# Kernel tuning notes

Measured on AMD Instinct MI355X. Metric: run time of the kernel, lower is better.

Reference implementation:

```python
import jax, jax.numpy as jnp
import numpy as np
from jax import lax

EPS = 1e-12

V, D, L, B = 50000, 128, 2048, 64
K1, K2 = 64, 64
W1, W2, W3 = 8, 8, 8


def conv1d_same(x, w):
    # x: [B, L, Cin], w: [W, Cin, Cout] -> [B, L, Cout]
    return lax.conv_general_dilated(x, w, window_strides=(1,), padding='SAME',
                                    dimension_numbers=('NWC', 'WIO', 'NWC'))


def gru_final_state(x, Wx, Wh, b):
    # Keras GRU (reset_after=True, gate order z, r, h); returns final hidden state.
    # x: [B, L, D] -> h_T: [B, K2]
    U = Wh.shape[0]
    x_proj = jnp.einsum('bld,dk->blk', x, Wx) + b[0]  # [B, L, 3U]

    def step(h, xp_t):
        hp = h @ Wh + b[1]                       # [B, 3U]
        xz, xr, xh = jnp.split(xp_t, 3, axis=-1)
        hz, hr, hh_ = jnp.split(hp, 3, axis=-1)
        z = jax.nn.sigmoid(xz + hz)
        r = jax.nn.sigmoid(xr + hr)
        hh = jnp.tanh(xh + r * hh_)
        h_new = z * h + (1.0 - z) * hh
        return h_new, None

    h0 = jnp.zeros((x.shape[0], U), dtype=x.dtype)
    h_T, _ = lax.scan(step, h0, jnp.swapaxes(x_proj, 0, 1))
    return h_T


def setup_inputs() -> dict:
    key = jax.random.key(0)
    ks = jax.random.split(key, 10)
    s = 0.05
    return {
        'code_block': jax.random.randint(ks[0], (B, L), 0, V, dtype=jnp.int32),
        'E': jax.random.normal(ks[1], (V, D), jnp.float32) * s,
        'bias_table': jax.random.normal(ks[2], (V, 1), jnp.float32) * s,
        'Wx': jax.random.normal(ks[3], (D, 3 * K2), jnp.float32) * s,
        'Wh': jax.random.normal(ks[4], (K2, 3 * K2), jnp.float32) * s,
        'b_gru': jnp.zeros((2, 3 * K2), jnp.float32),
        'c1w': jax.random.normal(ks[5], (W1, D, K1), jnp.float32) * s,
        'c1b': jnp.zeros((K1,), jnp.float32),
        'c2w': jax.random.normal(ks[6], (W2, K1, K2), jnp.float32) * s,
        'c2b': jnp.zeros((K2,), jnp.float32),
        'c3w': jax.random.normal(ks[7], (W3, K2, 1), jnp.float32) * s,
        'c3b': jnp.zeros((1,), jnp.float32),
    }


def reference(code_block, E, bias_table, Wx, Wh, b_gru, c1w, c1b, c2w, c2b, c3w, c3b):
    tok = E[code_block]                          # [B, L, D] embedding gather
    bias = bias_table[code_block][..., 0]        # [B, L] per-token bias

    h_t = gru_final_state(tok, Wx, Wh, b_gru)    # [B, K2]

    # AttentionFeatures: conv -> relu -> conv -> * h_t -> l2-normalize (dropout off)
    L1 = jax.nn.relu(conv1d_same(tok, c1w) + c1b)        # [B, L, K1]
    L2 = (conv1d_same(L1, c2w) + c2b) * h_t[:, None, :]  # [B, L, K2]
    L_feat = L2 * lax.rsqrt(jnp.sum(L2 * L2, axis=-1, keepdims=True) + EPS)

    # AttentionWeights: conv to 1 channel, softmax over time
    a_logits = conv1d_same(L_feat, c3w)[..., 0] + c3b    # [B, L]
    alpha = jax.nn.softmax(a_logits, axis=-1)            # [B, L]

    # n_hat = sum_l alpha_l * embed_l
    n_hat = jnp.einsum('bl,bld->bd', alpha, tok)         # [B, D]

    # logits_l = <embed_l, n_hat> + bias_l ; softmax over positions
    logits = jnp.einsum('bld,bd->bl', tok, n_hat) + bias # [B, L]
    return jax.nn.softmax(logits, axis=-1)
```

## Files before the change

### kernel.cpp

```cpp
#include <hip/hip_runtime.h>

#define B_ 64
#define L_ 2048
#define D_ 128
#define LP 2056
#define PAD 3

typedef __attribute__((ext_vector_type(8))) short short8;
typedef __attribute__((ext_vector_type(4))) float f32x4;
typedef __attribute__((ext_vector_type(4))) unsigned short us4;

static __device__ __forceinline__ float bf2f(unsigned short u) {
  return __uint_as_float(((unsigned int)u) << 16);
}
static __device__ __forceinline__ unsigned short f2bf(float f) {
  unsigned int x = __float_as_uint(f);
  unsigned int r = (x + 0x7fffu + ((x >> 16) & 1u)) >> 16;
  return (unsigned short)r;
}

__global__ __launch_bounds__(256) void k_prep(
    const int* __restrict__ code, const float* __restrict__ bias_table,
    const float* __restrict__ Wx, const float* __restrict__ c1w,
    const float* __restrict__ c2w,
    unsigned short* __restrict__ tokpad, unsigned short* __restrict__ WxT,
    unsigned short* __restrict__ c1wT, unsigned short* __restrict__ c2wT,
    float* __restrict__ biasg)
{
  int id = blockIdx.x * 256 + threadIdx.x;
  const int NB = B_ * L_;
  if (id < NB) { biasg[id] = bias_table[code[id]]; return; }
  id -= NB;
  const int N3 = 192 * 128;
  if (id < N3) { int c = id >> 7, d = id & 127; WxT[id] = f2bf(Wx[d * 192 + c]); return; }
  id -= N3;
  const int N4 = 8 * 64 * 128;
  if (id < N4) {
    int w = id >> 13, c = (id >> 7) & 63, d = id & 127;
    c1wT[id] = f2bf(c1w[(w * 128 + d) * 64 + c]); return;
  }
  id -= N4;
  const int N5 = 8 * 64 * 64;
  if (id < N5) {
    int w = id >> 12, c = (id >> 6) & 63, d = id & 63;
    c2wT[id] = f2bf(c2w[(w * 64 + d) * 64 + c]); return;
  }
  id -= N5;
  if (id < 8192) {
    int b = id >> 7, rem = id & 127;
    int rr = rem >> 4, c8 = rem & 15;
    int row = (rr < 3) ? rr : (2051 + rr - 3);
    uint4 z = {0u, 0u, 0u, 0u};
    ((uint4*)tokpad)[(b * LP + row) * 16 + c8] = z;
  }
}

__global__ __launch_bounds__(256) void k_xproj(
    const int* __restrict__ code, const float* __restrict__ E,
    const unsigned short* __restrict__ WxT, const float* __restrict__ bg,
    unsigned short* __restrict__ tokpad, unsigned short* __restrict__ xg)
{
  __shared__ __align__(16) unsigned short At[128 * 136];
  __shared__ __align__(16) unsigned short Bt[192 * 136];
  __shared__ int codes[128];
  int b = blockIdx.x >> 4;
  int l0 = (blockIdx.x & 15) << 7;
  int tid = threadIdx.x;
  if (tid < 128) codes[tid] = code[b * L_ + l0 + tid];
  __syncthreads();
  for (int i = tid; i < 128 * 16; i += 256) {
    int row = i >> 4, c8 = i & 15;
    const float4* e = (const float4*)(E + (size_t)codes[row] * D_ + c8 * 8);
    float4 e0 = e[0], e1 = e[1];
    uint4 o;
    o.x = f2bf(e0.x) | ((unsigned int)f2bf(e0.y) << 16);
    o.y = f2bf(e0.z) | ((unsigned int)f2bf(e0.w) << 16);
    o.z = f2bf(e1.x) | ((unsigned int)f2bf(e1.y) << 16);
    o.w = f2bf(e1.z) | ((unsigned int)f2bf(e1.w) << 16);
    *((uint4*)&At[row * 136 + c8 * 8]) = o;
    ((uint4*)tokpad)[(b * LP + PAD + l0 + row) * 16 + c8] = o;
  }
  for (int i = tid; i < 192 * 16; i += 256) {
    int row = i >> 4, c8 = i & 15;
    uint4 v = ((const uint4*)WxT)[i];
    *((uint4*)&Bt[row * 136 + c8 * 8]) = v;
  }
  __syncthreads();
  int wave = tid >> 6, lane = tid & 63;
  int m = lane & 15, q = lane >> 4;
  f32x4 acc[2][12];
  #pragma unroll
  for (int mt = 0; mt < 2; ++mt)
    #pragma unroll
    for (int nt = 0; nt < 12; ++nt) acc[mt][nt] = (f32x4){0.f,0.f,0.f,0.f};
  #pragma unroll
  for (int ks = 0; ks < 4; ++ks) {
    int kof = ks * 32 + q * 8;
    short8 a[2], bb[12];
    #pragma unroll
    for (int mt = 0; mt < 2; ++mt)
      a[mt] = *(const short8*)&At[(wave * 32 + mt * 16 + m) * 136 + kof];
    #pragma unroll
    for (int nt = 0; nt < 12; ++nt)
      bb[nt] = *(const short8*)&Bt[(nt * 16 + m) * 136 + kof];
    #pragma unroll
    for (int mt = 0; mt < 2; ++mt)
      #pragma unroll
      for (int nt = 0; nt < 12; ++nt)
        acc[mt][nt] = __builtin_amdgcn_mfma_f32_16x16x32_bf16(a[mt], bb[nt], acc[mt][nt], 0, 0, 0);
  }
  __syncthreads();
  #pragma unroll
  for (int mt = 0; mt < 2; ++mt) {
    int lrow = wave * 32 + mt * 16 + q * 4;
    #pragma unroll
    for (int nt = 0; nt < 12; ++nt) {
      int c = nt * 16 + m;
      float b0 = bg[c];
      us4 val;
      val.x = f2bf(acc[mt][nt][0] + b0);
      val.y = f2bf(acc[mt][nt][1] + b0);
      val.z = f2bf(acc[mt][nt][2] + b0);
      val.w = f2bf(acc[mt][nt][3] + b0);
      *((us4*)&Bt[c * 136 + lrow]) = val;
    }
  }
  __syncthreads();
  for (int i = tid; i < 64 * 32; i += 256) {
    int j = i >> 5, g = i & 31;
    us4 z4 = *(const us4*)&Bt[j * 136 + g * 4];
    us4 r4 = *(const us4*)&Bt[(64 + j) * 136 + g * 4];
    us4 h4 = *(const us4*)&Bt[(128 + j) * 136 + g * 4];
    uint4 o0, o1;
    o0.x = (unsigned)z4.x | ((unsigned)r4.x << 16); o0.y = (unsigned)h4.x;
    o0.z = (unsigned)z4.y | ((unsigned)r4.y << 16); o0.w = (unsigned)h4.y;
    o1.x = (unsigned)z4.z | ((unsigned)r4.z << 16); o1.y = (unsigned)h4.z;
    o1.z = (unsigned)z4.w | ((unsigned)r4.w << 16); o1.w = (unsigned)h4.w;
    size_t stp = (size_t)(b * 64 + j) * L_ + l0 + g * 4;
    ((uint4*)xg)[stp >> 1]       = o0;
    ((uint4*)xg)[(stp >> 1) + 1] = o1;
  }
}

#define BARRIER() asm volatile("s_waitcnt lgkmcnt(0)\n\ts_barrier" ::: "memory")

__global__ __launch_bounds__(192)
__attribute__((amdgpu_waves_per_eu(1, 1)))
void k_fused(
    const unsigned short* __restrict__ xg, const float* __restrict__ Wh,
    const float* __restrict__ bg, float* __restrict__ h_t,
    const unsigned short* __restrict__ tokpad,
    const unsigned short* __restrict__ c1wT, const float* __restrict__ c1b,
    const unsigned short* __restrict__ c2wT, const float* __restrict__ c2b,
    unsigned short* __restrict__ c2o)
{
  __shared__ __align__(16) unsigned short pool[39744];
  int bid = blockIdx.x;
  int tid = threadIdx.x;

  if (bid < 64) {
    int w = tid >> 6, j = tid & 63;
    float* xch = (float*)pool;
    int b = bid;
    int kb = w * 22;

    float wz[22], wr[22], wh[22];
    #pragma unroll
    for (int i = 0; i < 22; ++i) {
      int k = kb + i;
      bool ok = k < 64;
      wz[i] = ok ? Wh[k * 192 + j]       : 0.f;
      wr[i] = ok ? Wh[k * 192 + 64 + j]  : 0.f;
      wh[i] = ok ? Wh[k * 192 + 128 + j] : 0.f;
    }
    #pragma unroll
    for (int i = 0; i < 22; ++i)
      asm volatile("" : "+v"(wz[i]), "+v"(wr[i]), "+v"(wh[i]));

    float seedz = (w == 0) ? bg[192 + j]       : 0.f;
    float seedr = (w == 0) ? bg[192 + 64 + j]  : 0.f;
    float seedh = (w == 0) ? bg[192 + 128 + j] : 0.f;
    float hreg = 0.f;

    const uint4* xp = (const uint4*)(xg + (size_t)(b * 64 + j) * L_ * 4);
    uint4 cur_ = xp[0];
    uint4 nxt_ = xp[1];

#define STEP(WZR, WH_, P) { \
    float hk[22]; \
    _Pragma("unroll") \
    for (int i = 0; i < 22; ++i) \
      hk[i] = __int_as_float(__builtin_amdgcn_readlane(__float_as_int(hreg), (kb + i) & 63)); \
    __builtin_amdgcn_sched_barrier(0); \
    float az[4] = {seedz, 0.f, 0.f, 0.f}; \
    float ar[4] = {seedr, 0.f, 0.f, 0.f}; \
    float ah[4] = {seedh, 0.f, 0.f, 0.f}; \
    _Pragma("unroll") \
    for (int i = 0; i < 22; ++i) { \
      az[i & 3] = fmaf(hk[i], wz[i], az[i & 3]); \
      ar[i & 3] = fmaf(hk[i], wr[i], ar[i & 3]); \
      ah[i & 3] = fmaf(hk[i], wh[i], ah[i & 3]); \
    } \
    float4 pv; \
    pv.x = (az[0] + az[1]) + (az[2] + az[3]); \
    pv.y = (ar[0] + ar[1]) + (ar[2] + ar[3]); \
    pv.z = (ah[0] + ah[1]) + (ah[2] + ah[3]); \
    pv.w = 0.f; \
    *((float4*)&xch[(P) * 768 + (w * 64 + j) * 4]) = pv; \
    BARRIER(); \
    float4 q0 = *((const float4*)&xch[(P) * 768 + (0 * 64 + j) * 4]); \
    float4 q1 = *((const float4*)&xch[(P) * 768 + (1 * 64 + j) * 4]); \
    float4 q2 = *((const float4*)&xch[(P) * 768 + (2 * 64 + j) * 4]); \
    float sz = (q0.x + q1.x) + q2.x; \
    float sr = (q0.y + q1.y) + q2.y; \
    float sh = (q0.z + q1.z) + q2.z; \
    float xvz = bf2f((unsigned short)((WZR) & 0xffffu)); \
    float xvr = bf2f((unsigned short)((WZR) >> 16)); \
    float xvh = bf2f((unsigned short)((WH_) & 0xffffu)); \
    float zg = 1.f / (1.f + __expf(-(xvz + sz))); \
    float rg = 1.f / (1.f + __expf(-(xvr + sr))); \
    float e2 = __expf(-2.f * (xvh + rg * sh)); \
    float hh = fmaf(2.f, __frcp_rn(1.f + e2), -1.f); \
    hreg = zg * hreg + (1.f - zg) * hh; \
  }

    #pragma nounroll
    for (int p = 0; p < L_ / 2; ++p) {
      int pn = (p < L_ / 2 - 2) ? p + 2 : (L_ / 2 - 1);
      uint4 nn = xp[pn];
      STEP(cur_.x, cur_.y, 0)
      STEP(cur_.z, cur_.w, 1)
      cur_ = nxt_; nxt_ = nn;
    }
#undef STEP
    if (w == 0) h_t[b * 64 + j] = hreg;
    return;
  }

  unsigned short* At    = pool;
  unsigned short* l1buf = pool + 20672;
  unsigned short* Bw    = pool + 31040;
  int wv = tid >> 6, lane = tid & 63;
  int m = lane & 15, q = lane >> 4;

  for (int job = bid - 64; job < 1024; job += 192) {
    int b = job >> 4;
    int l0 = (job & 15) << 7;
    __syncthreads();
    for (int i = tid; i < 152 * 16; i += 192) {
      int row = i >> 4, c8 = i & 15;
      int p = l0 - 3 + row;
      p = p < 0 ? 0 : (p > 2055 ? 2055 : p);
      *((uint4*)&At[row * 136 + c8 * 8]) = ((const uint4*)tokpad)[(b * LP + p) * 16 + c8];
    }
    f32x4 acc[3][4];
    #pragma unroll
    for (int mt = 0; mt < 3; ++mt)
      #pragma unroll
      for (int nt = 0; nt < 4; ++nt) acc[mt][nt] = (f32x4){0.f,0.f,0.f,0.f};
    for (int w8 = 0; w8 < 8; ++w8) {
      __syncthreads();
      for (int i = tid; i < 64 * 16; i += 192) {
        int row = i >> 4, c8 = i & 15;
        *((uint4*)&Bw[row * 136 + c8 * 8]) = ((const uint4*)c1wT)[(w8 * 64 + row) * 16 + c8];
      }
      __syncthreads();
      #pragma unroll
      for (int ks = 0; ks < 4; ++ks) {
        int kof = ks * 32 + q * 8;
        short8 a[3], bb[4];
        #pragma unroll
        for (int mt = 0; mt < 3; ++mt) {
          int tl = wv + 3 * mt;
          a[mt] = *(const short8*)&At[(tl * 16 + m + w8) * 136 + kof];
        }
        #pragma unroll
        for (int nt = 0; nt < 4; ++nt)
          bb[nt] = *(const short8*)&Bw[(nt * 16 + m) * 136 + kof];
        #pragma unroll
        for (int mt = 0; mt < 3; ++mt)
          #pragma unroll
          for (int nt = 0; nt < 4; ++nt)
            acc[mt][nt] = __builtin_amdgcn_mfma_f32_16x16x32_bf16(a[mt], bb[nt], acc[mt][nt], 0, 0, 0);
      }
    }
    #pragma unroll
    for (int mt = 0; mt < 3; ++mt) {
      int tl = wv + 3 * mt;
      #pragma unroll
      for (int nt = 0; nt < 4; ++nt) {
        int c = nt * 16 + m;
        float bs = c1b[c];
        #pragma unroll
        for (int r = 0; r < 4; ++r) {
          float v = fmaxf(acc[mt][nt][r] + bs, 0.f);
          l1buf[(tl * 16 + q * 4 + r) * 72 + c] = f2bf(v);
        }
      }
    }
    __syncthreads();
    for (int i2 = tid; i2 < 135 * 8; i2 += 192) {
      int i = i2 >> 3, c8 = i2 & 7;
      int jrow = l0 - 3 + i;
      if (jrow < 0 || jrow > 2047) {
        uint4 z4 = {0u,0u,0u,0u};
        *((uint4*)&l1buf[i * 72 + c8 * 8]) = z4;
      }
    }
    f32x4 acc2[3][4];
    #pragma unroll
    for (int mt = 0; mt < 3; ++mt)
      #pragma unroll
      for (int nt = 0; nt < 4; ++nt) acc2[mt][nt] = (f32x4){0.f,0.f,0.f,0.f};
    for (int w8 = 0; w8 < 8; ++w8) {
      __syncthreads();
      for (int i = tid; i < 64 * 8; i += 192) {
        int row = i >> 3, c8 = i & 7;
        *((uint4*)&Bw[row * 72 + c8 * 8]) = ((const uint4*)c2wT)[(w8 * 64 + row) * 8 + c8];
      }
      __syncthreads();
      #pragma unroll
      for (int ks = 0; ks < 2; ++ks) {
        int kof = ks * 32 + q * 8;
        short8 a[3], bb[4];
        #pragma unroll
        for (int mt = 0; mt < 3; ++mt) {
          int tl = wv + 3 * mt;
          if (tl < 8)
            a[mt] = *(const short8*)&l1buf[(tl * 16 + m + w8) * 72 + kof];
        }
        #pragma unroll
        for (int nt = 0; nt < 4; ++nt)
          bb[nt] = *(const short8*)&Bw[(nt * 16 + m) * 72 + kof];
        #pragma unroll
        for (int mt = 0; mt < 3; ++mt) {
          int tl = wv + 3 * mt;
          if (tl < 8)
            #pragma unroll
            for (int nt = 0; nt < 4; ++nt)
              acc2[mt][nt] = __builtin_amdgcn_mfma_f32_16x16x32_bf16(a[mt], bb[nt], acc2[mt][nt], 0, 0, 0);
        }
      }
    }
    #pragma unroll
    for (int mt = 0; mt < 3; ++mt) {
      int tl = wv + 3 * mt;
      if (tl < 8) {
        #pragma unroll
        for (int nt = 0; nt < 4; ++nt) {
          int c = nt * 16 + m;
          float bs = c2b[c];
          #pragma unroll
          for (int r = 0; r < 4; ++r)
            c2o[(size_t)(b * L_ + l0 + tl * 16 + q * 4 + r) * 64 + c] = f2bf(acc2[mt][nt][r] + bs);
        }
      }
    }
  }
}

__global__ __launch_bounds__(256) void k_alpha(
    const unsigned short* __restrict__ c2o, const float* __restrict__ h_t,
    const float* __restrict__ c3w, const float* __restrict__ c3b,
    float* __restrict__ a_out)
{
  __shared__ float Lf[71 * 65];
  __shared__ float red[256];
  __shared__ float ht[64];
  __shared__ float c3[512];
  int b = blockIdx.x >> 5;
  int tile = blockIdx.x & 31;
  int tid = threadIdx.x, lane = tid & 63, wave = tid >> 6;
  if (tid < 64) ht[tid] = h_t[b * 64 + tid];
  for (int i = tid; i < 512; i += 256) c3[i] = c3w[i];
  float c3bias = c3b[0];
  __syncthreads();
  int lt = tile << 6;
  for (int i0 = wave; i0 < 71; i0 += 4) {
    int l = lt - 3 + i0;
    float v = 0.f;
    if (l >= 0 && l < L_) v = bf2f(c2o[((size_t)b * L_ + l) * 64 + lane]) * ht[lane];
    float ss = v * v;
    #pragma unroll
    for (int msk = 1; msk < 64; msk <<= 1) ss += __shfl_xor(ss, msk);
    Lf[i0 * 65 + lane] = v * rsqrtf(ss + 1e-12f);
  }
  __syncthreads();
  {
    int u = lane, part = wave;
    float p = 0.f;
    #pragma unroll
    for (int w = 0; w < 8; ++w)
      #pragma unroll
      for (int cc = 0; cc < 16; ++cc) {
        int c = part * 16 + cc;
        p += Lf[(u + w) * 65 + c] * c3[w * 64 + c];
      }
    red[tid] = p;
  }
  __syncthreads();
  if (tid < 64)
    a_out[b * L_ + lt + tid] = red[tid] + red[64 + tid] + red[128 + tid] + red[192 + tid] + c3bias;
}

__global__ __launch_bounds__(256) void k_soft1(float* __restrict__ a)
{
  __shared__ float a_lds[2048];
  __shared__ float red[256];
  int b = blockIdx.x, tid = threadIdx.x, lane = tid & 63, wave = tid >> 6;
  for (int i = tid; i < 2048; i += 256) a_lds[i] = a[b * L_ + i];
  __syncthreads();
  float mx = -1e30f;
  for (int i = tid; i < 2048; i += 256) mx = fmaxf(mx, a_lds[i]);
  #pragma unroll
  for (int msk = 1; msk < 64; msk <<= 1) mx = fmaxf(mx, __shfl_xor(mx, msk));
  if (lane == 0) red[wave] = mx;
  __syncthreads();
  mx = fmaxf(fmaxf(red[0], red[1]), fmaxf(red[2], red[3]));
  float sm = 0.f;
  for (int i = tid; i < 2048; i += 256) sm += __expf(a_lds[i] - mx);
  #pragma unroll
  for (int msk = 1; msk < 64; msk <<= 1) sm += __shfl_xor(sm, msk);
  __syncthreads();
  if (lane == 0) red[wave] = sm;
  __syncthreads();
  sm = red[0] + red[1] + red[2] + red[3];
  float inv = 1.f / sm;
  for (int i = tid; i < 2048; i += 256) a[b * L_ + i] = __expf(a_lds[i] - mx) * inv;
}

__global__ __launch_bounds__(256) void k_nhat(
    const unsigned short* __restrict__ tokpad, const float* __restrict__ alpha,
    float* __restrict__ npart)
{
  __shared__ float nred[512];
  int b = blockIdx.x >> 3, c = blockIdx.x & 7;
  int tid = threadIdx.x;
  int d2 = tid & 63, g = tid >> 6;
  int l0 = c << 8;
  float ax = 0.f, ay = 0.f;
  for (int i = 0; i < 64; ++i) {
    int l = l0 + g + 4 * i;
    unsigned int uu = *(const unsigned int*)&tokpad[((size_t)b * LP + PAD + l) * 128 + d2 * 2];
    float al = alpha[b * L_ + l];
    ax += al * bf2f((unsigned short)(uu & 0xffffu));
    ay += al * bf2f((unsigned short)(uu >> 16));
  }
  nred[g * 128 + d2 * 2] = ax;
  nred[g * 128 + d2 * 2 + 1] = ay;
  __syncthreads();
  if (tid < 128)
    npart[((b << 3) + c) * 128 + tid] = nred[tid] + nred[128 + tid] + nred[256 + tid] + nred[384 + tid];
}

__global__ __launch_bounds__(256) void k_logits(
    const unsigned short* __restrict__ tokpad, const float* __restrict__ npart,
    const float* __restrict__ biasg, float* __restrict__ l_all)
{
  __shared__ float nhat[128];
  int b = blockIdx.x >> 3, c = blockIdx.x & 7;
  int tid = threadIdx.x;
  if (tid < 128) {
    const float* p = npart + (b << 3) * 128 + tid;
    nhat[tid] = ((p[0] + p[128]) + (p[256] + p[384]))
              + ((p[512] + p[640]) + (p[768] + p[896]));
  }
  __syncthreads();
  int l = (c << 8) + tid;
  const uint4* rowp = (const uint4*)&tokpad[((size_t)b * LP + PAD + l) * 128];
  float s = 0.f;
  #pragma unroll
  for (int jj = 0; jj < 16; ++jj) {
    uint4 uu = rowp[jj];
    s += bf2f((unsigned short)(uu.x & 0xffffu)) * nhat[jj*8+0]
       + bf2f((unsigned short)(uu.x >> 16))     * nhat[jj*8+1]
       + bf2f((unsigned short)(uu.y & 0xffffu)) * nhat[jj*8+2]
       + bf2f((unsigned short)(uu.y >> 16))     * nhat[jj*8+3]
       + bf2f((unsigned short)(uu.z & 0xffffu)) * nhat[jj*8+4]
       + bf2f((unsigned short)(uu.z >> 16))     * nhat[jj*8+5]
       + bf2f((unsigned short)(uu.w & 0xffffu)) * nhat[jj*8+6]
       + bf2f((unsigned short)(uu.w >> 16))     * nhat[jj*8+7];
  }
  l_all[b * L_ + l] = s + biasg[b * L_ + l];
}

__global__ __launch_bounds__(256) void k_soft2(
    const float* __restrict__ l_all, float* __restrict__ out)
{
  __shared__ float l_lds[2048];
  __shared__ float red[256];
  int b = blockIdx.x, tid = threadIdx.x, lane = tid & 63, wave = tid >> 6;
  for (int i = tid; i < 2048; i += 256) l_lds[i] = l_all[b * L_ + i];
  __syncthreads();
  float mx = -1e30f;
  for (int i = tid; i < 2048; i += 256) mx = fmaxf(mx, l_lds[i]);
  #pragma unroll
  for (int msk = 1; msk < 64; msk <<= 1) mx = fmaxf(mx, __shfl_xor(mx, msk));
  __syncthreads();
  if (lane == 0) red[wave] = mx;
  __syncthreads();
  mx = fmaxf(fmaxf(red[0], red[1]), fmaxf(red[2], red[3]));
  float sm = 0.f;
  for (int i = tid; i < 2048; i += 256) sm += __expf(l_lds[i] - mx);
  #pragma unroll
  for (int msk = 1; msk < 64; msk <<= 1) sm += __shfl_xor(sm, msk);
  __syncthreads();
  if (lane == 0) red[wave] = sm;
  __syncthreads();
  sm = red[0] + red[1] + red[2] + red[3];
  float inv = 1.f / sm;
  for (int i = tid; i < 2048; i += 256) out[b * L_ + i] = __expf(l_lds[i] - mx) * inv;
}

extern "C" void kernel_launch(void* const* d_in, const int* in_sizes, int n_in,
                              void* d_out, int out_size, void* d_ws, size_t ws_size,
                              hipStream_t stream) {
  const int*   code = (const int*)d_in[0];
  const float* E    = (const float*)d_in[1];
  const float* bt   = (const float*)d_in[2];
  const float* Wx   = (const float*)d_in[3];
  const float* Wh   = (const float*)d_in[4];
  const float* bg   = (const float*)d_in[5];
  const float* c1w  = (const float*)d_in[6];
  const float* c1b  = (const float*)d_in[7];
  const float* c2w  = (const float*)d_in[8];
  const float* c2b  = (const float*)d_in[9];
  const float* c3w  = (const float*)d_in[10];
  const float* c3b  = (const float*)d_in[11];
  char* ws = (char*)d_ws;
  unsigned short* tokpad = (unsigned short*)(ws);
  unsigned short* xg     = (unsigned short*)(ws + 33685504);
  unsigned short* c2o    = (unsigned short*)(ws + 100794368);
  unsigned short* WxT    = (unsigned short*)(ws + 117571584);
  unsigned short* c1wT   = (unsigned short*)(ws + 117620736);
  unsigned short* c2wT   = (unsigned short*)(ws + 117751808);
  float*          htp    = (float*)(ws + 117817344);
  float*          biasg  = (float*)(ws + 117833728);
  float*          alog   = (float*)(ws + 33685504);
  float*          npart  = (float*)(ws + 33685504 + 1048576);
  float*          l_all  = (float*)(ws + 33685504 + 2097152);

  k_prep  <<<1024, 256, 0, stream>>>(code, bt, Wx, c1w, c2w, tokpad, WxT, c1wT, c2wT, biasg);
  k_xproj <<<1024, 256, 0, stream>>>(code, E, WxT, bg, tokpad, xg);
  k_fused <<<256, 192, 0, stream>>>(xg, Wh, bg, htp, tokpad, c1wT, c1b, c2wT, c2b, c2o);
  k_alpha <<<2048, 256, 0, stream>>>(c2o, htp, c3w, c3b, alog);
  k_soft1 <<<64, 256, 0, stream>>>(alog);
  k_nhat  <<<512, 256, 0, stream>>>(tokpad, alog, npart);
  k_logits<<<512, 256, 0, stream>>>(tokpad, npart, biasg, l_all);
  k_soft2 <<<64, 256, 0, stream>>>(l_all, (float*)d_out);
}
```

Baseline: 1.079 ms.

## Fuse attention softmax into n_hat and logits into final softmax kernel

The first softmax is folded into k_nhat: each of the 8 chunk blocks per batch row recomputes the row max and sum from the logits and derives alpha on the fly, so the separate softmax kernel and its write-back go away. The logits dot product is merged with the final softmax into one block per batch row, which keeps logits in LDS instead of writing them to global memory. This removes two launches and some global traffic. In exchange the softmax reductions are repeated 8 times per row, and the logits stage drops from 512 blocks to 64, which cuts parallelism for the token-row reads.

```diff
diff --git a/kernel.cpp b/kernel.cpp
--- a/kernel.cpp
+++ b/kernel.cpp
@@ -403,12 +403,16 @@
     a_out[b * L_ + lt + tid] = red[tid] + red[64 + tid] + red[128 + tid] + red[192 + tid] + c3bias;
 }
 
-__global__ __launch_bounds__(256) void k_soft1(float* __restrict__ a)
+__global__ __launch_bounds__(256) void k_nhat(
+    const unsigned short* __restrict__ tokpad, const float* __restrict__ alog,
+    float* __restrict__ npart)
 {
   __shared__ float a_lds[2048];
   __shared__ float red[256];
-  int b = blockIdx.x, tid = threadIdx.x, lane = tid & 63, wave = tid >> 6;
-  for (int i = tid; i < 2048; i += 256) a_lds[i] = a[b * L_ + i];
+  __shared__ float nred[512];
+  int b = blockIdx.x >> 3, c = blockIdx.x & 7;
+  int tid = threadIdx.x, lane = tid & 63, wave = tid >> 6;
+  for (int i = tid; i < 2048; i += 256) a_lds[i] = alog[b * L_ + i];
   __syncthreads();
   float mx = -1e30f;
   for (int i = tid; i < 2048; i += 256) mx = fmaxf(mx, a_lds[i]);
@@ -426,23 +430,13 @@
   __syncthreads();
   sm = red[0] + red[1] + red[2] + red[3];
   float inv = 1.f / sm;
-  for (int i = tid; i < 2048; i += 256) a[b * L_ + i] = __expf(a_lds[i] - mx) * inv;
-}
-
-__global__ __launch_bounds__(256) void k_nhat(
-    const unsigned short* __restrict__ tokpad, const float* __restrict__ alpha,
-    float* __restrict__ npart)
-{
-  __shared__ float nred[512];
-  int b = blockIdx.x >> 3, c = blockIdx.x & 7;
-  int tid = threadIdx.x;
   int d2 = tid & 63, g = tid >> 6;
   int l0 = c << 8;
   float ax = 0.f, ay = 0.f;
   for (int i = 0; i < 64; ++i) {
     int l = l0 + g + 4 * i;
     unsigned int uu = *(const unsigned int*)&tokpad[((size_t)b * LP + PAD + l) * 128 + d2 * 2];
-    float al = alpha[b * L_ + l];
+    float al = __expf(a_lds[l] - mx) * inv;
     ax += al * bf2f((unsigned short)(uu & 0xffffu));
     ay += al * bf2f((unsigned short)(uu >> 16));
   }
@@ -455,42 +449,37 @@
 
 __global__ __launch_bounds__(256) void k_logits(
     const unsigned short* __restrict__ tokpad, const float* __restrict__ npart,
-    const float* __restrict__ biasg, float* __restrict__ l_all)
+    const float* __restrict__ biasg, float* __restrict__ out)
 {
   __shared__ float nhat[128];
-  int b = blockIdx.x >> 3, c = blockIdx.x & 7;
-  int tid = threadIdx.x;
+  __shared__ float l_lds[2048];
+  __shared__ float red[256];
+  int b = blockIdx.x;
+  int tid = threadIdx.x, lane = tid & 63, wave = tid >> 6;
   if (tid < 128) {
     const float* p = npart + (b << 3) * 128 + tid;
     nhat[tid] = ((p[0] + p[128]) + (p[256] + p[384]))
               + ((p[512] + p[640]) + (p[768] + p[896]));
   }
   __syncthreads();
-  int l = (c << 8) + tid;
-  const uint4* rowp = (const uint4*)&tokpad[((size_t)b * LP + PAD + l) * 128];
-  float s = 0.f;
-  #pragma unroll
-  for (int jj = 0; jj < 16; ++jj) {
-    uint4 uu = rowp[jj];
-    s += bf2f((unsigned short)(uu.x & 0xffffu)) * nhat[jj*8+0]
-       + bf2f((unsigned short)(uu.x >> 16))     * nhat[jj*8+1]
-       + bf2f((unsigned short)(uu.y & 0xffffu)) * nhat[jj*8+2]
-       + bf2f((unsigned short)(uu.y >> 16))     * nhat[jj*8+3]
-       + bf2f((unsigned short)(uu.z & 0xffffu)) * nhat[jj*8+4]
-       + bf2f((unsigned short)(uu.z >> 16))     * nhat[jj*8+5]
-       + bf2f((unsigned short)(uu.w & 0xffffu)) * nhat[jj*8+6]
-       + bf2f((unsigned short)(uu.w >> 16))     * nhat[jj*8+7];
-  }
-  l_all[b * L_ + l] = s + biasg[b * L_ + l];
-}
-
-__global__ __launch_bounds__(256) void k_soft2(
-    const float* __restrict__ l_all, float* __restrict__ out)
-{
-  __shared__ float l_lds[2048];
-  __shared__ float red[256];
-  int b = blockIdx.x, tid = threadIdx.x, lane = tid & 63, wave = tid >> 6;
-  for (int i = tid; i < 2048; i += 256) l_lds[i] = l_all[b * L_ + i];
+  for (int li = 0; li < 8; ++li) {
+    int l = li * 256 + tid;
+    const uint4* rowp = (const uint4*)&tokpad[((size_t)b * LP + PAD + l) * 128];
+    float s = 0.f;
+    #pragma unroll
+    for (int jj = 0; jj < 16; ++jj) {
+      uint4 uu = rowp[jj];
+      s += bf2f((unsigned short)(uu.x & 0xffffu)) * nhat[jj*8+0]
+         + bf2f((unsigned short)(uu.x >> 16))     * nhat[jj*8+1]
+         + bf2f((unsigned short)(uu.y & 0xffffu)) * nhat[jj*8+2]
+         + bf2f((unsigned short)(uu.y >> 16))     * nhat[jj*8+3]
+         + bf2f((unsigned short)(uu.z & 0xffffu)) * nhat[jj*8+4]
+         + bf2f((unsigned short)(uu.z >> 16))     * nhat[jj*8+5]
+         + bf2f((unsigned short)(uu.w & 0xffffu)) * nhat[jj*8+6]
+         + bf2f((unsigned short)(uu.w >> 16))     * nhat[jj*8+7];
+    }
+    l_lds[l] = s + biasg[b * L_ + l];
+  }
   __syncthreads();
   float mx = -1e30f;
   for (int i = tid; i < 2048; i += 256) mx = fmaxf(mx, l_lds[i]);
@@ -538,14 +527,11 @@
   float*          biasg  = (float*)(ws + 117833728);
   float*          alog   = (float*)(ws + 33685504);
   float*          npart  = (float*)(ws + 33685504 + 1048576);
-  float*          l_all  = (float*)(ws + 33685504 + 2097152);
 
   k_prep  <<<1024, 256, 0, stream>>>(code, bt, Wx, c1w, c2w, tokpad, WxT, c1wT, c2wT, biasg);
   k_xproj <<<1024, 256, 0, stream>>>(code, E, WxT, bg, tokpad, xg);
   k_fused <<<256, 192, 0, stream>>>(xg, Wh, bg, htp, tokpad, c1wT, c1b, c2wT, c2b, c2o);
   k_alpha <<<2048, 256, 0, stream>>>(c2o, htp, c3w, c3b, alog);
-  k_soft1 <<<64, 256, 0, stream>>>(alog);
   k_nhat  <<<512, 256, 0, stream>>>(tokpad, alog, npart);
-  k_logits<<<512, 256, 0, stream>>>(tokpad, npart, biasg, l_all);
-  k_soft2 <<<64, 256, 0, stream>>>(l_all, (float*)d_out);
-}
+  k_logits<<<64, 256, 0, stream>>>(tokpad, npart, biasg, (float*)d_out);
+}
```

Result: no change. 1.092 ms (+1.2%).
